# Kernel optimization log

Hardware: AMD Instinct MI355X
Metric: run time of the kernel (lower is better)

## Reference

```python
import jax, jax.numpy as jnp
import numpy as np

EMB_DIM = 128
DEC_DIM = 128
NEG_INF = -1e10


def setup_inputs() -> dict:
    key = jax.random.key(0)
    k1, k2, k3, k4, k5, k6 = jax.random.split(key, 6)
    B, S = 64, 4096
    hidden = jax.random.normal(k1, (B, DEC_DIM), dtype=jnp.float32)
    seq_embs = jax.random.normal(k2, (S, B, EMB_DIM), dtype=jnp.float32)
    mask = jax.random.randint(k3, (B, S), 0, 2, dtype=jnp.int32)
    # nn.Linear(emb_dim + dec_dim, dec_dim): weight [dec_dim, emb_dim+dec_dim]
    fan_in = EMB_DIM + DEC_DIM
    bound = 1.0 / np.sqrt(fan_in)
    W_attn = jax.random.uniform(k4, (DEC_DIM, fan_in), minval=-bound, maxval=bound, dtype=jnp.float32)
    b_attn = jax.random.uniform(k5, (DEC_DIM,), minval=-bound, maxval=bound, dtype=jnp.float32)
    # nn.Linear(dec_dim, 1, bias=False): weight [1, dec_dim]
    bound_v = 1.0 / np.sqrt(DEC_DIM)
    v_w = jax.random.uniform(k6, (1, DEC_DIM), minval=-bound_v, maxval=bound_v, dtype=jnp.float32)
    return {"hidden": hidden, "seq_embs": seq_embs, "mask": mask,
            "W_attn": W_attn, "b_attn": b_attn, "v_w": v_w}


def reference(hidden, seq_embs, mask, W_attn, b_attn, v_w):
    # hidden: [B, Dd]; seq_embs: [S, B, De]; mask: [B, S]
    # Concat order in torch is (hidden, seq_embs) -> split W accordingly.
    Wh = W_attn[:, :DEC_DIM]   # [Dd, Dd] applied to hidden
    We = W_attn[:, DEC_DIM:]   # [Dd, De] applied to seq_embs
    embs = jnp.transpose(seq_embs, (1, 0, 2))            # [B, S, De]
    # energy = tanh(Linear(cat(hidden, embs))) without materializing concat
    h_proj = hidden @ Wh.T + b_attn                       # [B, Dd]
    e_proj = jnp.einsum('bse,de->bsd', embs, We)          # [B, S, Dd]
    energy = jnp.tanh(h_proj[:, None, :] + e_proj)        # [B, S, Dd]
    attention = jnp.einsum('bsd,d->bs', energy, v_w[0])   # [B, S]
    attention = jnp.where(mask == 0, NEG_INF, attention)
    return jax.nn.softmax(attention, axis=1)
```

## Files before the change

kernel.cpp:

```cpp
#include <hip/hip_runtime.h>
#include <hip/hip_bf16.h>

#define BB 64
#define SS 4096
#define EE 128
#define DD 128
#define FAN 256
#define TILES 2
#define ROWS (TILES * 64)
#define NEG_INF_F (-1e10f)

typedef __bf16 bf16x8 __attribute__((ext_vector_type(8)));
typedef unsigned short u16x8 __attribute__((ext_vector_type(8)));
typedef float f32x4 __attribute__((ext_vector_type(4)));

__device__ inline bf16x8 ld_frag_lds(const unsigned char* p) {
    union { u16x8 u; bf16x8 b; } c;
    c.u = *(const u16x8*)p;
    return c.b;
}

__device__ inline uint2 f4_to_bf4(float4 f) {
    union { __hip_bfloat162 b; unsigned u; } lo, hi;
    lo.b = __float22bfloat162_rn(make_float2(f.x, f.y));
    hi.b = __float22bfloat162_rn(make_float2(f.z, f.w));
    return make_uint2(lo.u, hi.u);
}

__device__ inline float tanh_fast(float x) {
    float ax = fabsf(x);
    float e = __expf(-2.0f * ax);
    float t = (1.0f - e) * __builtin_amdgcn_rcpf(1.0f + e);
    return x < 0.0f ? -t : t;
}

__global__ __launch_bounds__(256) void prep_kernel(
        const float* __restrict__ hidden, const float* __restrict__ W_attn,
        const float* __restrict__ b_attn, const float* __restrict__ v_w,
        float* __restrict__ hproj, unsigned char* __restrict__ Wb,
        float* __restrict__ v_out, float* __restrict__ sums) {
    const int b = blockIdx.x;
    const int t = threadIdx.x;
    if (t == 0) sums[b] = 0.0f;
    if (t < 128) {
        float acc = b_attn[t];
        const float4* hrow = (const float4*)(hidden + b * DD);
        const float4* wrow = (const float4*)(W_attn + t * FAN);
        #pragma unroll
        for (int e = 0; e < 32; e++) {
            float4 h = hrow[e], w = wrow[e];
            acc += h.x * w.x + h.y * w.y + h.z * w.z + h.w * w.w;
        }
        hproj[b * DD + t] = acc;
        if (b == 0) v_out[t] = v_w[t];
    } else {
        int tt = t - 128;
        int d  = 2 * b + (tt >> 6);
        int e0 = (tt & 63) * 2;
        float2 src = *(const float2*)(W_attn + d * FAN + DD + e0);
        union { __hip_bfloat162 bb; unsigned u; } c;
        c.bb = __float22bfloat162_rn(src);
        unsigned off = (unsigned)(d * 256)
                     + (((unsigned)(e0 * 2)) ^ (((unsigned)d & 7u) << 4));
        *(unsigned*)(Wb + off) = c.u;
    }
}

__global__ __launch_bounds__(256, 4) void logits_kernel(
        const float* __restrict__ seq_embs, const int* __restrict__ mask,
        const float* __restrict__ hproj, const unsigned char* __restrict__ Wb,
        const float* __restrict__ v, float* __restrict__ out,
        float* __restrict__ sums) {
    __shared__ __attribute__((aligned(1024))) unsigned char Ws[DD * EE * 2];

    const int b    = blockIdx.y;
    const int g    = blockIdx.x;
    const int tid  = threadIdx.x;
    const int wave = tid >> 6;
    const int lane = tid & 63;
    const int m    = lane & 15;
    const int quad = lane >> 4;

    #pragma unroll
    for (int j = 0; j < 8; j++) {
        const int c = wave * 8 + j;
        __builtin_amdgcn_global_load_lds(
            (const __attribute__((address_space(1))) unsigned int*)(Wb + c * 1024 + lane * 16),
            (__attribute__((address_space(3))) unsigned int*)(Ws + c * 1024),
            16, 0, 0);
    }

    const int* __restrict__ mask_g = mask + (size_t)b * SS + g * ROWS;
    int  am[TILES];
    int4 mq[TILES];
    bf16x8 af[TILES][4];
    const float* __restrict__ xb = seq_embs
        + (size_t)(g * ROWS + wave * 16 + m) * (BB * EE)
        + (size_t)b * EE + quad * 8;
    #pragma unroll
    for (int tl = 0; tl < TILES; tl++) {
        am[tl] = mask_g[tl * 64 + wave * 16 + m];
        mq[tl] = *(const int4*)(mask_g + tl * 64 + wave * 16 + quad * 4);
        const float* xr = xb + (size_t)(tl * 64) * (BB * EE);
        #pragma unroll
        for (int kk = 0; kk < 4; kk++) {
            union { uint4 q; bf16x8 bf; } cc;
            cc.q = make_uint4(0u, 0u, 0u, 0u);
            if (am[tl] != 0) {
                float4 f0 = *(const float4*)(xr + kk * 32);
                float4 f1 = *(const float4*)(xr + kk * 32 + 4);
                uint2 a = f4_to_bf4(f0), bq = f4_to_bf4(f1);
                cc.q = make_uint4(a.x, a.y, bq.x, bq.y);
            }
            af[tl][kk] = cc.bf;
        }
    }

    float hp_r[8], v_r[8];
    #pragma unroll
    for (int t = 0; t < 8; t++) {
        hp_r[t] = hproj[b * DD + t * 16 + m];
        v_r[t]  = v[t * 16 + m];
    }

    __syncthreads();

    float part[TILES][4];
    #pragma unroll
    for (int tl = 0; tl < TILES; tl++)
        #pragma unroll
        for (int r = 0; r < 4; r++) part[tl][r] = 0.0f;

    const unsigned sw = ((unsigned)(m & 7)) << 4;
    #pragma unroll
    for (int t = 0; t < 8; t++) {
        const unsigned rbase = (unsigned)((t * 16 + m) * 256);
        bf16x8 bf[4];
        #pragma unroll
        for (int kk = 0; kk < 4; kk++) {
            const unsigned cb = ((unsigned)(kk * 64 + quad * 16)) ^ sw;
            bf[kk] = ld_frag_lds(Ws + rbase + cb);
        }
        #pragma unroll
        for (int tl = 0; tl < TILES; tl++) {
            f32x4 acc = (f32x4){0.f, 0.f, 0.f, 0.f};
            #pragma unroll
            for (int kk = 0; kk < 4; kk++)
                acc = __builtin_amdgcn_mfma_f32_16x16x32_bf16(af[tl][kk], bf[kk], acc, 0, 0, 0);
            #pragma unroll
            for (int r = 0; r < 4; r++)
                part[tl][r] += v_r[t] * tanh_fast(hp_r[t] + acc[r]);
        }
    }

    float blocksum = 0.0f;
    #pragma unroll
    for (int tl = 0; tl < TILES; tl++) {
        const int mqa[4] = {mq[tl].x, mq[tl].y, mq[tl].z, mq[tl].w};
        float red[4];
        #pragma unroll
        for (int r = 0; r < 4; r++) {
            float p = part[tl][r];
            p += __shfl_xor(p, 1);
            p += __shfl_xor(p, 2);
            p += __shfl_xor(p, 4);
            p += __shfl_xor(p, 8);
            red[r] = (mqa[r] != 0) ? __expf(p) : 0.0f;
            blocksum += red[r];
        }
        if (m == 0) {
            *(float4*)&out[(size_t)b * SS + g * ROWS + tl * 64 + wave * 16 + quad * 4] =
                make_float4(red[0], red[1], red[2], red[3]);
        }
    }
    blocksum += __shfl_xor(blocksum, 16);
    blocksum += __shfl_xor(blocksum, 32);
    if (lane == 0) atomicAdd(&sums[b], blocksum);
}

__global__ __launch_bounds__(256) void norm_kernel(
        float* __restrict__ out, const float* __restrict__ sums) {
    const int b = blockIdx.y;
    const float inv = 1.0f / sums[b];
    const int i = (blockIdx.x * 256 + threadIdx.x) * 4;
    float4 v = *(float4*)&out[(size_t)b * SS + i];
    v.x *= inv; v.y *= inv; v.z *= inv; v.w *= inv;
    *(float4*)&out[(size_t)b * SS + i] = v;
}

extern "C" void kernel_launch(void* const* d_in, const int* in_sizes, int n_in,
                              void* d_out, int out_size, void* d_ws, size_t ws_size,
                              hipStream_t stream) {
    const float* hidden   = (const float*)d_in[0];
    const float* seq_embs = (const float*)d_in[1];
    const int*   mask     = (const int*)d_in[2];
    const float* W_attn   = (const float*)d_in[3];
    const float* b_attn   = (const float*)d_in[4];
    const float* v_w      = (const float*)d_in[5];
    float* out = (float*)d_out;

    float*         hproj = (float*)d_ws;
    unsigned char* Wb    = (unsigned char*)d_ws + 32768;
    float*         vv    = (float*)((char*)d_ws + 65536);
    float*         sums  = (float*)((char*)d_ws + 66048);

    prep_kernel<<<64, 256, 0, stream>>>(hidden, W_attn, b_attn, v_w, hproj, Wb, vv, sums);
    dim3 grid(SS / ROWS, BB);
    logits_kernel<<<grid, 256, 0, stream>>>(seq_embs, mask, hproj, Wb, vv, out, sums);
    dim3 ngrid(SS / (256 * 4), BB);
    norm_kernel<<<ngrid, 256, 0, stream>>>(out, sums);
}
```

Before: 261.6 us.

## Double-buffer activation tiles and skip tanh for masked rows

```diff
diff --git a/kernel.cpp b/kernel.cpp
--- a/kernel.cpp
+++ b/kernel.cpp
@@ -6,7 +6,7 @@
 #define EE 128
 #define DD 128
 #define FAN 256
-#define TILES 2
+#define TILES 4
 #define ROWS (TILES * 64)
 #define NEG_INF_F (-1e10f)
 
@@ -80,6 +80,7 @@
     const int lane = tid & 63;
     const int m    = lane & 15;
     const int quad = lane >> 4;
+    const int arow = wave * 16 + m;
 
     #pragma unroll
     for (int j = 0; j < 8; j++) {
@@ -91,28 +92,28 @@
     }
 
     const int* __restrict__ mask_g = mask + (size_t)b * SS + g * ROWS;
-    int  am[TILES];
-    int4 mq[TILES];
-    bf16x8 af[TILES][4];
-    const float* __restrict__ xb = seq_embs
-        + (size_t)(g * ROWS + wave * 16 + m) * (BB * EE)
+    const float* __restrict__ xbase = seq_embs
+        + (size_t)(g * ROWS + arow) * (BB * EE)
         + (size_t)b * EE + quad * 8;
-    #pragma unroll
-    for (int tl = 0; tl < TILES; tl++) {
-        am[tl] = mask_g[tl * 64 + wave * 16 + m];
-        mq[tl] = *(const int4*)(mask_g + tl * 64 + wave * 16 + quad * 4);
-        const float* xr = xb + (size_t)(tl * 64) * (BB * EE);
+
+    int am[2];
+    int4 mq[2];
+    bf16x8 af[2][4];
+    {
+        am[0] = mask_g[arow];
+        mq[0] = *(const int4*)(mask_g + wave * 16 + quad * 4);
+        const float* xrow = xbase;
         #pragma unroll
         for (int kk = 0; kk < 4; kk++) {
-            union { uint4 q; bf16x8 bf; } cc;
-            cc.q = make_uint4(0u, 0u, 0u, 0u);
-            if (am[tl] != 0) {
-                float4 f0 = *(const float4*)(xr + kk * 32);
-                float4 f1 = *(const float4*)(xr + kk * 32 + 4);
+            union { uint4 q; bf16x8 bf; } c;
+            c.q = make_uint4(0u, 0u, 0u, 0u);
+            if (am[0] != 0) {
+                float4 f0 = *(const float4*)(xrow + kk * 32);
+                float4 f1 = *(const float4*)(xrow + kk * 32 + 4);
                 uint2 a = f4_to_bf4(f0), bq = f4_to_bf4(f1);
-                cc.q = make_uint4(a.x, a.y, bq.x, bq.y);
-            }
-            af[tl][kk] = cc.bf;
+                c.q = make_uint4(a.x, a.y, bq.x, bq.y);
+            }
+            af[0][kk] = c.bf;
         }
     }
 
@@ -125,54 +126,70 @@
 
     __syncthreads();
 
-    float part[TILES][4];
+    const unsigned sw = ((unsigned)(m & 7)) << 4;
+    float blocksum = 0.0f;
+
     #pragma unroll
-    for (int tl = 0; tl < TILES; tl++)
-        #pragma unroll
-        for (int r = 0; r < 4; r++) part[tl][r] = 0.0f;
-
-    const unsigned sw = ((unsigned)(m & 7)) << 4;
-    #pragma unroll
-    for (int t = 0; t < 8; t++) {
-        const unsigned rbase = (unsigned)((t * 16 + m) * 256);
-        bf16x8 bf[4];
+    for (int tile = 0; tile < TILES; tile++) {
+        const int cur = tile & 1;
+        if (tile + 1 < TILES) {
+            const int nxt = cur ^ 1;
+            am[nxt] = mask_g[(tile + 1) * 64 + arow];
+            mq[nxt] = *(const int4*)(mask_g + (tile + 1) * 64 + wave * 16 + quad * 4);
+            const float* xrow = xbase + (size_t)((tile + 1) * 64) * (BB * EE);
+            #pragma unroll
+            for (int kk = 0; kk < 4; kk++) {
+                union { uint4 q; bf16x8 bf; } c;
+                c.q = make_uint4(0u, 0u, 0u, 0u);
+                if (am[nxt] != 0) {
+                    float4 f0 = *(const float4*)(xrow + kk * 32);
+                    float4 f1 = *(const float4*)(xrow + kk * 32 + 4);
+                    uint2 a = f4_to_bf4(f0), bq = f4_to_bf4(f1);
+                    c.q = make_uint4(a.x, a.y, bq.x, bq.y);
+                }
+                af[nxt][kk] = c.bf;
+            }
+        }
+
+        f32x4 acc[8];
+        #pragma unroll
+        for (int t = 0; t < 8; t++) acc[t] = (f32x4){0.f, 0.f, 0.f, 0.f};
         #pragma unroll
         for (int kk = 0; kk < 4; kk++) {
             const unsigned cb = ((unsigned)(kk * 64 + quad * 16)) ^ sw;
-            bf[kk] = ld_frag_lds(Ws + rbase + cb);
-        }
-        #pragma unroll
-        for (int tl = 0; tl < TILES; tl++) {
-            f32x4 acc = (f32x4){0.f, 0.f, 0.f, 0.f};
             #pragma unroll
-            for (int kk = 0; kk < 4; kk++)
-                acc = __builtin_amdgcn_mfma_f32_16x16x32_bf16(af[tl][kk], bf[kk], acc, 0, 0, 0);
-            #pragma unroll
-            for (int r = 0; r < 4; r++)
-                part[tl][r] += v_r[t] * tanh_fast(hp_r[t] + acc[r]);
-        }
-    }
-
-    float blocksum = 0.0f;
-    #pragma unroll
-    for (int tl = 0; tl < TILES; tl++) {
-        const int mqa[4] = {mq[tl].x, mq[tl].y, mq[tl].z, mq[tl].w};
+            for (int t = 0; t < 8; t++) {
+                bf16x8 bf = ld_frag_lds(Ws + (unsigned)((t * 16 + m) * 256) + cb);
+                acc[t] = __builtin_amdgcn_mfma_f32_16x16x32_bf16(af[cur][kk], bf, acc[t], 0, 0, 0);
+            }
+        }
+
+        const int mqa[4] = {mq[cur].x, mq[cur].y, mq[cur].z, mq[cur].w};
         float red[4];
         #pragma unroll
         for (int r = 0; r < 4; r++) {
-            float p = part[tl][r];
-            p += __shfl_xor(p, 1);
-            p += __shfl_xor(p, 2);
-            p += __shfl_xor(p, 4);
-            p += __shfl_xor(p, 8);
-            red[r] = (mqa[r] != 0) ? __expf(p) : 0.0f;
-            blocksum += red[r];
+            float red_r = 0.0f;
+            if (mqa[r] != 0) {
+                float part = 0.f;
+                #pragma unroll
+                for (int t = 0; t < 8; t++)
+                    part += v_r[t] * tanh_fast(hp_r[t] + acc[t][r]);
+                part += __shfl_xor(part, 1);
+                part += __shfl_xor(part, 2);
+                part += __shfl_xor(part, 4);
+                part += __shfl_xor(part, 8);
+                red_r = __expf(part);
+            }
+            red[r] = red_r;
+            blocksum += red_r;
         }
         if (m == 0) {
-            *(float4*)&out[(size_t)b * SS + g * ROWS + tl * 64 + wave * 16 + quad * 4] =
+            *(float4*)&out[(size_t)b * SS + g * ROWS + tile * 64
+                           + wave * 16 + quad * 4] =
                 make_float4(red[0], red[1], red[2], red[3]);
         }
     }
+
     blocksum += __shfl_xor(blocksum, 16);
     blocksum += __shfl_xor(blocksum, 32);
     if (lane == 0) atomicAdd(&sums[b], blocksum);
```

New measurement: 228.5 us. -12.6%, faster.
